# Optimization experiments

Measured on AMD Instinct MI355X. Metric: run time of the kernel, lower is better.

## Reference

```python
import jax, jax.numpy as jnp
import numpy as np

B = 8            # graphs per batch
NP = 1000        # nodes per graph (fixed 1000x1000 connectivity)
N = B * NP       # total nodes
F = 1000         # node feature dim (== NP)
HC = 32          # hidden_channels
NL = 3           # num_layers (HC*NL == 96, the hard-coded bnh dim)
K = 5            # Chebyshev order
HID = 128        # mlp hidden
NC = 2           # num_classes
DEG = 10         # avg degree
E = N * DEG      # total edges
TRI = F * (F - 1) // 2   # 499500 strict-upper-triangle entries
EPS = 1e-5


def setup_inputs():
    ks = jax.random.split(jax.random.key(0), 16)
    x = jax.random.normal(ks[0], (N, F), jnp.float32)  # per-graph connectivity rows
    # block-structured edges: endpoints stay inside their own graph
    offs = jnp.repeat(jnp.arange(B, dtype=jnp.int32) * NP, NP * DEG)
    src = jax.random.randint(ks[1], (E,), 0, NP, jnp.int32) + offs
    dst = jax.random.randint(ks[2], (E,), 0, NP, jnp.int32) + offs
    edge_index = jnp.stack([src, dst])
    batch = jnp.repeat(jnp.arange(B, dtype=jnp.int32), NP)
    nrm = lambda k, shape, s=0.05: jax.random.normal(k, shape, jnp.float32) * s
    return dict(
        x=x, edge_index=edge_index, batch=batch,
        conv_w0=nrm(ks[3], (K, F, HC)), conv_b0=jnp.zeros((HC,), jnp.float32),
        conv_w1=nrm(ks[4], (K, HC, HC)), conv_b1=jnp.zeros((HC,), jnp.float32),
        conv_w2=nrm(ks[5], (K, HC, HC)), conv_b2=jnp.zeros((HC,), jnp.float32),
        bnh_g=jnp.ones((HC * NL,), jnp.float32), bnh_b=jnp.zeros((HC * NL,), jnp.float32),
        bn_g=jnp.ones((TRI,), jnp.float32), bn_b=jnp.zeros((TRI,), jnp.float32),
        mlp_w1=nrm(ks[6], (TRI, HID), 0.002), mlp_b1=jnp.zeros((HID,), jnp.float32),
        bn1_g=jnp.ones((HID,), jnp.float32), bn1_b=jnp.zeros((HID,), jnp.float32),
        mlp_w2=nrm(ks[7], (HID, HID // 2)), mlp_b2=jnp.zeros((HID // 2,), jnp.float32),
        bn2_g=jnp.ones((HID // 2,), jnp.float32), bn2_b=jnp.zeros((HID // 2,), jnp.float32),
        mlp_w3=nrm(ks[8], (HID // 2, HID // 2)), mlp_b3=jnp.zeros((HID // 2,), jnp.float32),
        bn3_g=jnp.ones((HID // 2,), jnp.float32), bn3_b=jnp.zeros((HID // 2,), jnp.float32),
        mlp_w4=nrm(ks[9], (HID // 2, NC)), mlp_b4=jnp.zeros((NC,), jnp.float32),
    )


def _bn(z, g, b):
    # BatchNorm1d in training mode (batch stats, biased var), eps=1e-5
    m = jnp.mean(z, axis=0)
    v = jnp.var(z, axis=0)
    return (z - m) * jax.lax.rsqrt(v + EPS) * g + b


def _cheb(z, src, dst, w, Ws, b):
    # PyG ChebConv with sym norm, lambda_max=2: L~ = -D^{-1/2} A D^{-1/2}
    prop = lambda t: jax.ops.segment_sum(w[:, None] * t[src], dst, num_segments=N)
    Tx0, out = z, z @ Ws[0]
    Tx1 = prop(z)
    out = out + Tx1 @ Ws[1]
    for k in range(2, Ws.shape[0]):
        Tx2 = 2.0 * prop(Tx1) - Tx0
        out = out + Tx2 @ Ws[k]
        Tx0, Tx1 = Tx1, Tx2
    return out + b


def reference(x, edge_index, batch, conv_w0, conv_b0, conv_w1, conv_b1, conv_w2, conv_b2,
              bnh_g, bnh_b, bn_g, bn_b, mlp_w1, mlp_b1, bn1_g, bn1_b,
              mlp_w2, mlp_b2, bn2_g, bn2_b, mlp_w3, mlp_b3, bn3_g, bn3_b, mlp_w4, mlp_b4):
    src, dst = edge_index[0], edge_index[1]
    # symmetric normalization weights (negated scaled Laplacian off-diagonal)
    deg = jax.ops.segment_sum(jnp.ones((E,), x.dtype), src, num_segments=N)
    dinv = jnp.where(deg > 0, deg ** -0.5, 0.0)
    w = -dinv[src] * dinv[dst]
    # node features replaced by tiled identity, as in the original forward
    xid = jnp.tile(jnp.eye(NP, dtype=x.dtype), (B, 1))  # [N, F]
    h1 = jnp.tanh(_cheb(xid, src, dst, w, conv_w0, conv_b0))
    h2 = jnp.tanh(_cheb(h1, src, dst, w, conv_w1, conv_b1))
    h3 = jnp.tanh(_cheb(h2, src, dst, w, conv_w2, conv_b2))
    # MeanAggregation per graph
    cnt = jax.ops.segment_sum(jnp.ones((N,), x.dtype), batch, num_segments=B)[:, None]
    pool = lambda h: jax.ops.segment_sum(h, batch, num_segments=B) / cnt
    emb = jnp.concatenate([pool(h1), pool(h2), pool(h3)], axis=1)  # [B, 96]
    hbn = _bn(emb, bnh_g, bnh_b)
    # static strict-upper-triangle gather (replaces per-graph triu().nonzero())
    rawx = x.reshape(B, F, F)
    iu0, iu1 = np.triu_indices(F, k=1)
    feats = rawx[:, iu0, iu1]                       # [B, 499500]
    fbn = _bn(feats, bn_g, bn_b)
    # MLP (dropout = identity / eval)
    a = jax.nn.relu(_bn(fbn @ mlp_w1 + mlp_b1, bn1_g, bn1_b))
    a = jax.nn.relu(_bn(a @ mlp_w2 + mlp_b2, bn2_g, bn2_b))
    a = jax.nn.relu(_bn(a @ mlp_w3 + mlp_b3, bn3_g, bn3_b))
    logits = a @ mlp_w4 + mlp_b4
    logp = jax.nn.log_softmax(logits, axis=1)
    return logp, hbn
```

## Files before the change

### kernel.cpp

```cpp
#include <hip/hip_runtime.h>

#define NN 8000
#define NPP 1000
#define FF 1000
#define HCC 32
#define KK 5
#define EE 80000
#define EDGB 10000
#define DPAD 40
#define TRIN 499500
#define HID 128
#define EPSV 1e-5f
#define NREP 64

#define IDX_ACC  0
#define IDX_DEGI 65536
#define IDX_FILL 73536
#define IDX_OVC  81536
#define IDX_OVF  81540
#define IDX_EPAD 81920
#define ZERO_N   737280
#define IDX_H1   737280
#define IDX_H2   993280
#define IDX_EMB  1249280


__global__ void k_count(const int* __restrict__ src, int* __restrict__ degi) {
  int e = blockIdx.x * blockDim.x + threadIdx.x;
  if (e >= EE) return;
  atomicAdd(&degi[src[e]], 1);
}

__global__ void k_fillpad(const int* __restrict__ src, const int* __restrict__ dst,
                          const int* __restrict__ degi, int* __restrict__ fill,
                          int2* __restrict__ epad, int* __restrict__ ovc,
                          int4* __restrict__ ovf) {
  int e = blockIdx.x * blockDim.x + threadIdx.x;
  if (e >= EE) return;
  int s = src[e], d = dst[e];
  int dd = degi[d];
  float w = -rsqrtf((float)degi[s]) * ((dd > 0) ? rsqrtf((float)dd) : 0.0f);
  int g = e / EDGB;
  int sl = s - g * NPP;
  int dl = d - g * NPP;
  int pos = atomicAdd(&fill[d], 1);
  if (pos < DPAD) {
    int2 pk;
    pk.x = sl;
    pk.y = __float_as_int(w);
    epad[(size_t)g * (DPAD * 1024) + pos * 1024 + dl] = pk;
  } else {
    int oi = atomicAdd(ovc, 1);
    if (oi < 64) ovf[oi] = make_int4(g, dl, sl, __float_as_int(w));
  }
}

__global__ void __launch_bounds__(1024, 4) k_layer(
    const float* __restrict__ cw, const float* __restrict__ bias,
    const float* __restrict__ hin, float* __restrict__ hout,
    const int2* __restrict__ epad, const int* __restrict__ ovc,
    const int4* __restrict__ ovf,
    float* __restrict__ emb, int L) {
  __shared__ float ckl[KK][NPP];
  __shared__ float bcur[NPP];
  __shared__ float wcol[KK][HCC];
  __shared__ float part[32];
  const int t = threadIdx.x;
  const int g = blockIdx.x >> 5;
  const int c = blockIdx.x & 31;
  const bool act = t < NPP;
  if (hin == nullptr) {
    if (act) {
#pragma unroll
      for (int k = 0; k < KK; ++k)
        ckl[k][t] = cw[k * (FF * HCC) + t * HCC + c];
    }
  } else {
    if (t < KK * HCC) {
      int k = t >> 5, j = t & 31;
      wcol[k][j] = cw[k * (HCC * HCC) + j * HCC + c];
    }
    __syncthreads();
    if (act) {
      float hrow[HCC];
      const float* hp = hin + ((size_t)g * NPP + t) * HCC;
#pragma unroll
      for (int q = 0; q < HCC / 4; ++q) {
        float4 f = *(const float4*)(hp + q * 4);
        hrow[q * 4 + 0] = f.x; hrow[q * 4 + 1] = f.y;
        hrow[q * 4 + 2] = f.z; hrow[q * 4 + 3] = f.w;
      }
#pragma unroll
      for (int k = 0; k < KK; ++k) {
        float a = 0.0f;
#pragma unroll
        for (int j = 0; j < HCC; ++j) a += hrow[j] * wcol[k][j];
        ckl[k][t] = a;
      }
    }
  }
  __syncthreads();
  if (act) bcur[t] = ckl[KK - 1][t];
  float bprev = 0.0f;
  float v = 0.0f;
  __syncthreads();
  const int2* ed = epad + (size_t)g * (DPAD * 1024);
  const int nov = ovc[0];
#pragma unroll
  for (int step = 0; step < 4; ++step) {
    const float alpha = (step == 3) ? 1.0f : 2.0f;
    const int kidx = 3 - step;
    float acc = 0.0f;
#pragma unroll 8
    for (int d = 0; d < DPAD; ++d) {
      int2 pk = ed[d * 1024 + t];
      acc += __int_as_float(pk.y) * bcur[pk.x];
    }
    for (int i = 0; i < nov; ++i) {
      int4 o = ovf[i];
      if (o.x == g && o.y == t) acc += __int_as_float(o.w) * bcur[o.z];
    }
    if (act) v = alpha * acc - bprev + ckl[kidx][t];
    __syncthreads();
    if (act) { bprev = bcur[t]; bcur[t] = v; }
    __syncthreads();
  }
  if (act) {
    float h = tanhf(v + bias[c]);
    if (hout) hout[((size_t)g * NPP + t) * HCC + c] = h;
    bcur[t] = h;
  }
  __syncthreads();
  if (t < 32) {
    float s = 0.0f;
    for (int i = t; i < NPP; i += 32) s += bcur[i];
    part[t] = s;
  }
  __syncthreads();
  if (t == 0) {
    float s = 0.0f;
#pragma unroll
    for (int q = 0; q < 32; ++q) s += part[q];
    emb[g * 96 + L * HCC + c] = s * (1.0f / (float)NPP);
  }
}


__device__ __forceinline__ int tri_S(int i) { return i * 999 - (i * (i - 1)) / 2; }

__global__ void __launch_bounds__(256) k_gemm1(const float* __restrict__ x,
                                               const float* __restrict__ bng,
                                               const float* __restrict__ bnb,
                                               const float* __restrict__ W1,
                                               float* __restrict__ accrep) {
  __shared__ float fbn_s[256][8];
  __shared__ float red[8][128];
  const int tid = threadIdx.x;
  const int c4 = (tid & 31) * 4;
  const int stripe = tid >> 5;
  const int j0 = blockIdx.x * 256;
  float acc[8][4];
#pragma unroll
  for (int b = 0; b < 8; ++b)
#pragma unroll
    for (int q = 0; q < 4; ++q) acc[b][q] = 0.0f;

  {
    const int j = j0 + tid;
    float vals[8];
    if (j < TRIN) {
      const float tt = 1999.0f;
      int i = (int)((tt - sqrtf(tt * tt - 8.0f * (float)j)) * 0.5f);
      i = max(0, min(i, 998));
      while (tri_S(i + 1) <= j) ++i;
      while (tri_S(i) > j) --i;
      int i1 = j - tri_S(i) + i + 1;
      size_t base = (size_t)i * FF + i1;
#pragma unroll
      for (int b = 0; b < 8; ++b) vals[b] = x[(size_t)b * (FF * NPP) + base];
      float m = 0.0f;
#pragma unroll
      for (int b = 0; b < 8; ++b) m += vals[b];
      m *= 0.125f;
      float va = 0.0f;
#pragma unroll
      for (int b = 0; b < 8; ++b) { float d = vals[b] - m; va += d * d; }
      va *= 0.125f;
      float sc = bng[j] * rsqrtf(va + EPSV);
      float tb = bnb[j] - m * sc;
#pragma unroll
      for (int b = 0; b < 8; ++b) vals[b] = sc * vals[b] + tb;
    } else {
#pragma unroll
      for (int b = 0; b < 8; ++b) vals[b] = 0.0f;
    }
    *(float4*)&fbn_s[tid][0] = make_float4(vals[0], vals[1], vals[2], vals[3]);
    *(float4*)&fbn_s[tid][4] = make_float4(vals[4], vals[5], vals[6], vals[7]);
  }
  __syncthreads();

  const int jbase = stripe * 32;
  const int jmax = min(32, TRIN - j0 - jbase);
  const float* wp = W1 + (size_t)(j0 + jbase) * HID + c4;
  if (jmax == 32) {
#pragma unroll 4
    for (int jj = 0; jj < 32; ++jj) {
      float4 w = *(const float4*)(wp + (size_t)jj * HID);
      float4 f0 = *(const float4*)&fbn_s[jbase + jj][0];
      float4 f1 = *(const float4*)&fbn_s[jbase + jj][4];
      float wv[4] = {w.x, w.y, w.z, w.w};
      float fv[8] = {f0.x, f0.y, f0.z, f0.w, f1.x, f1.y, f1.z, f1.w};
#pragma unroll
      for (int b = 0; b < 8; ++b)
#pragma unroll
        for (int q = 0; q < 4; ++q) acc[b][q] += fv[b] * wv[q];
    }
  } else {
    for (int jj = 0; jj < jmax; ++jj) {
      float4 w = *(const float4*)(wp + (size_t)jj * HID);
      float4 f0 = *(const float4*)&fbn_s[jbase + jj][0];
      float4 f1 = *(const float4*)&fbn_s[jbase + jj][4];
      float wv[4] = {w.x, w.y, w.z, w.w};
      float fv[8] = {f0.x, f0.y, f0.z, f0.w, f1.x, f1.y, f1.z, f1.w};
#pragma unroll
      for (int b = 0; b < 8; ++b)
#pragma unroll
        for (int q = 0; q < 4; ++q) acc[b][q] += fv[b] * wv[q];
    }
  }
#pragma unroll
  for (int b = 0; b < 8; ++b) {
    __syncthreads();
    red[stripe][c4 + 0] = acc[b][0];
    red[stripe][c4 + 1] = acc[b][1];
    red[stripe][c4 + 2] = acc[b][2];
    red[stripe][c4 + 3] = acc[b][3];
    __syncthreads();
    if (tid < 128) {
      float s = 0.0f;
#pragma unroll
      for (int q = 0; q < 8; ++q) s += red[q][tid];
      atomicAdd(&accrep[(blockIdx.x & (NREP - 1)) * 1024 + b * HID + tid], s);
    }
  }
}


__global__ void __launch_bounds__(1024) k_mlp(
    const float* __restrict__ accrep, const float* __restrict__ emb,
    const float* __restrict__ hg, const float* __restrict__ hb,
    const float* __restrict__ mb1,
    const float* __restrict__ g1, const float* __restrict__ be1,
    const float* __restrict__ W2, const float* __restrict__ mb2,
    const float* __restrict__ g2, const float* __restrict__ be2,
    const float* __restrict__ W3, const float* __restrict__ mb3,
    const float* __restrict__ g3, const float* __restrict__ be3,
    const float* __restrict__ W4, const float* __restrict__ mb4,
    float* __restrict__ out) {
  __shared__ float A[8][128];
  __shared__ float V[8][128];
  __shared__ float Bm[8][64];
  __shared__ float Cm[8][64];
  __shared__ float lg[8][2];
  const int tid = threadIdx.x;
  if (tid < 96) {
    float v[8];
    float m = 0.0f;
#pragma unroll
    for (int q = 0; q < 8; ++q) { v[q] = emb[q * 96 + tid]; m += v[q]; }
    m *= 0.125f;
    float va = 0.0f;
#pragma unroll
    for (int q = 0; q < 8; ++q) { float d = v[q] - m; va += d * d; }
    va *= 0.125f;
    float s = hg[tid] * rsqrtf(va + EPSV);
    float t = hb[tid] - m * s;
#pragma unroll
    for (int q = 0; q < 8; ++q) out[16 + q * 96 + tid] = s * v[q] + t;
  }
  {
    const int c = tid & 127;
    const int b = tid >> 7;
    float a = mb1[c];
#pragma unroll 8
    for (int rep = 0; rep < NREP; ++rep) a += accrep[rep * 1024 + tid];
    V[b][c] = a;
  }
  __syncthreads();
  {
    const int c = tid & 127;
    const int b = tid >> 7;
    float m = 0.0f;
#pragma unroll
    for (int q = 0; q < 8; ++q) m += V[q][c];
    m *= 0.125f;
    float va = 0.0f;
#pragma unroll
    for (int q = 0; q < 8; ++q) { float d = V[q][c] - m; va += d * d; }
    va *= 0.125f;
    float s = g1[c] * rsqrtf(va + EPSV);
    float t = be1[c] - m * s;
    float z = s * V[b][c] + t;
    A[b][c] = (z > 0.0f) ? z : 0.0f;
  }
  __syncthreads();
  if (tid < 512) {
    const int c = tid & 63;
    const int b = tid >> 6;
    float a = mb2[c];
    for (int j = 0; j < 128; ++j) a += A[b][j] * W2[j * 64 + c];
    V[b][c] = a;
  }
  __syncthreads();
  if (tid < 512) {
    const int c = tid & 63;
    const int b = tid >> 6;
    float m = 0.0f;
#pragma unroll
    for (int q = 0; q < 8; ++q) m += V[q][c];
    m *= 0.125f;
    float va = 0.0f;
#pragma unroll
    for (int q = 0; q < 8; ++q) { float d = V[q][c] - m; va += d * d; }
    va *= 0.125f;
    float s = g2[c] * rsqrtf(va + EPSV);
    float t = be2[c] - m * s;
    float z = s * V[b][c] + t;
    Bm[b][c] = (z > 0.0f) ? z : 0.0f;
  }
  __syncthreads();
  if (tid < 512) {
    const int c = tid & 63;
    const int b = tid >> 6;
    float a = mb3[c];
    for (int j = 0; j < 64; ++j) a += Bm[b][j] * W3[j * 64 + c];
    V[b][c] = a;
  }
  __syncthreads();
  if (tid < 512) {
    const int c = tid & 63;
    const int b = tid >> 6;
    float m = 0.0f;
#pragma unroll
    for (int q = 0; q < 8; ++q) m += V[q][c];
    m *= 0.125f;
    float va = 0.0f;
#pragma unroll
    for (int q = 0; q < 8; ++q) { float d = V[q][c] - m; va += d * d; }
    va *= 0.125f;
    float s = g3[c] * rsqrtf(va + EPSV);
    float t = be3[c] - m * s;
    float z = s * V[b][c] + t;
    Cm[b][c] = (z > 0.0f) ? z : 0.0f;
  }
  __syncthreads();
  if (tid < 16) {
    int b = tid >> 1, c = tid & 1;
    float a4 = mb4[c];
    for (int j = 0; j < 64; ++j) a4 += Cm[b][j] * W4[j * 2 + c];
    lg[b][c] = a4;
  }
  __syncthreads();
  if (tid < 8) {
    float l0 = lg[tid][0], l1 = lg[tid][1];
    float mm = fmaxf(l0, l1);
    float lse = mm + logf(expf(l0 - mm) + expf(l1 - mm));
    out[tid * 2 + 0] = l0 - lse;
    out[tid * 2 + 1] = l1 - lse;
  }
}


extern "C" void kernel_launch(void* const* d_in, const int* in_sizes, int n_in,
                              void* d_out, int out_size, void* d_ws, size_t ws_size,
                              hipStream_t stream) {
  const float* x = (const float*)d_in[0];
  const int* ei = (const int*)d_in[1];
  const int* src = ei;
  const int* dst = ei + EE;
  const float* cw0 = (const float*)d_in[3];
  const float* cb0 = (const float*)d_in[4];
  const float* cw1 = (const float*)d_in[5];
  const float* cb1 = (const float*)d_in[6];
  const float* cw2 = (const float*)d_in[7];
  const float* cb2 = (const float*)d_in[8];
  const float* bnhg = (const float*)d_in[9];
  const float* bnhb = (const float*)d_in[10];
  const float* bng = (const float*)d_in[11];
  const float* bnb = (const float*)d_in[12];
  const float* mw1 = (const float*)d_in[13];
  const float* mb1 = (const float*)d_in[14];
  const float* b1g = (const float*)d_in[15];
  const float* b1b = (const float*)d_in[16];
  const float* mw2 = (const float*)d_in[17];
  const float* mb2 = (const float*)d_in[18];
  const float* b2g = (const float*)d_in[19];
  const float* b2b = (const float*)d_in[20];
  const float* mw3 = (const float*)d_in[21];
  const float* mb3 = (const float*)d_in[22];
  const float* b3g = (const float*)d_in[23];
  const float* b3b = (const float*)d_in[24];
  const float* mw4 = (const float*)d_in[25];
  const float* mb4 = (const float*)d_in[26];

  float* ws = (float*)d_ws;
  int* wsi = (int*)d_ws;
  float* out = (float*)d_out;

  float* accrep = ws + IDX_ACC;
  int* degi = wsi + IDX_DEGI;
  int* fill = wsi + IDX_FILL;
  int* ovc = wsi + IDX_OVC;
  int4* ovf = (int4*)(wsi + IDX_OVF);
  int2* epad = (int2*)(wsi + IDX_EPAD);
  float* h1 = ws + IDX_H1;
  float* h2 = ws + IDX_H2;
  float* emb = ws + IDX_EMB;

  hipMemsetAsync(wsi, 0, ZERO_N * sizeof(int), stream);

  k_gemm1<<<(TRIN + 255) / 256, 256, 0, stream>>>(x, bng, bnb, mw1, accrep);
  k_count<<<(EE + 255) / 256, 256, 0, stream>>>(src, degi);
  k_fillpad<<<(EE + 255) / 256, 256, 0, stream>>>(src, dst, degi, fill, epad, ovc, ovf);
  k_layer<<<256, 1024, 0, stream>>>(cw0, cb0, nullptr, h1, epad, ovc, ovf, emb, 0);
  k_layer<<<256, 1024, 0, stream>>>(cw1, cb1, h1, h2, epad, ovc, ovf, emb, 1);
  k_layer<<<256, 1024, 0, stream>>>(cw2, cb2, h2, nullptr, epad, ovc, ovf, emb, 2);
  k_mlp<<<1, 1024, 0, stream>>>(accrep, emb, bnhg, bnhb, mb1, b1g, b1b,
                                mw2, mb2, b2g, b2b, mw3, mb3, b3g, b3b,
                                mw4, mb4, out);
}
```

Baseline: 524.0 us.

## Keep padded edge lists and Chebyshev coefficients in registers; shrink padding

Edge padding per destination drops from 40 to 24 slots, with a larger overflow buffer (256) for the rare nodes above that. Each thread now loads its padded edge list and Chebyshev coefficients into registers once and reuses them over all four recurrence steps, instead of reading global memory every step and keeping coefficients in shared memory. The launch bound is relaxed to 2 blocks per SM for the extra registers, and one barrier is dropped on the last step. Separately, the MLP weight stream uses nontemporal loads; the trade-off is lower occupancy and a longer linear scan of the overflow list each step if many nodes overflow.

```diff
diff --git a/kernel.cpp b/kernel.cpp
--- a/kernel.cpp
+++ b/kernel.cpp
@@ -7,22 +7,25 @@
 #define KK 5
 #define EE 80000
 #define EDGB 10000
-#define DPAD 40
+#define DPAD 24
+#define OVCAP 256
 #define TRIN 499500
 #define HID 128
 #define EPSV 1e-5f
 #define NREP 64
+
+typedef float fvec4 __attribute__((ext_vector_type(4)));
 
 #define IDX_ACC  0
 #define IDX_DEGI 65536
 #define IDX_FILL 73536
 #define IDX_OVC  81536
 #define IDX_OVF  81540
-#define IDX_EPAD 81920
-#define ZERO_N   737280
-#define IDX_H1   737280
-#define IDX_H2   993280
-#define IDX_EMB  1249280
+#define IDX_EPAD 82564
+#define ZERO_N   475780
+#define IDX_H1   475780
+#define IDX_H2   731780
+#define IDX_EMB  987780
 
 
 __global__ void k_count(const int* __restrict__ src, int* __restrict__ degi) {
@@ -51,17 +54,16 @@
     epad[(size_t)g * (DPAD * 1024) + pos * 1024 + dl] = pk;
   } else {
     int oi = atomicAdd(ovc, 1);
-    if (oi < 64) ovf[oi] = make_int4(g, dl, sl, __float_as_int(w));
-  }
-}
-
-__global__ void __launch_bounds__(1024, 4) k_layer(
+    if (oi < OVCAP) ovf[oi] = make_int4(g, dl, sl, __float_as_int(w));
+  }
+}
+
+__global__ void __launch_bounds__(1024, 2) k_layer(
     const float* __restrict__ cw, const float* __restrict__ bias,
     const float* __restrict__ hin, float* __restrict__ hout,
     const int2* __restrict__ epad, const int* __restrict__ ovc,
     const int4* __restrict__ ovf,
     float* __restrict__ emb, int L) {
-  __shared__ float ckl[KK][NPP];
   __shared__ float bcur[NPP];
   __shared__ float wcol[KK][HCC];
   __shared__ float part[32];
@@ -69,64 +71,65 @@
   const int g = blockIdx.x >> 5;
   const int c = blockIdx.x & 31;
   const bool act = t < NPP;
+  const int tn = act ? t : 0;
+  float ck[KK];
   if (hin == nullptr) {
-    if (act) {
-#pragma unroll
-      for (int k = 0; k < KK; ++k)
-        ckl[k][t] = cw[k * (FF * HCC) + t * HCC + c];
-    }
+#pragma unroll
+    for (int k = 0; k < KK; ++k)
+      ck[k] = cw[k * (FF * HCC) + tn * HCC + c];
   } else {
     if (t < KK * HCC) {
       int k = t >> 5, j = t & 31;
       wcol[k][j] = cw[k * (HCC * HCC) + j * HCC + c];
     }
     __syncthreads();
-    if (act) {
-      float hrow[HCC];
-      const float* hp = hin + ((size_t)g * NPP + t) * HCC;
-#pragma unroll
-      for (int q = 0; q < HCC / 4; ++q) {
-        float4 f = *(const float4*)(hp + q * 4);
-        hrow[q * 4 + 0] = f.x; hrow[q * 4 + 1] = f.y;
-        hrow[q * 4 + 2] = f.z; hrow[q * 4 + 3] = f.w;
-      }
-#pragma unroll
-      for (int k = 0; k < KK; ++k) {
-        float a = 0.0f;
-#pragma unroll
-        for (int j = 0; j < HCC; ++j) a += hrow[j] * wcol[k][j];
-        ckl[k][t] = a;
-      }
-    }
-  }
-  __syncthreads();
-  if (act) bcur[t] = ckl[KK - 1][t];
+    float hrow[HCC];
+    const float* hp = hin + ((size_t)g * NPP + tn) * HCC;
+#pragma unroll
+    for (int q = 0; q < HCC / 4; ++q) {
+      float4 f = *(const float4*)(hp + q * 4);
+      hrow[q * 4 + 0] = f.x; hrow[q * 4 + 1] = f.y;
+      hrow[q * 4 + 2] = f.z; hrow[q * 4 + 3] = f.w;
+    }
+#pragma unroll
+    for (int k = 0; k < KK; ++k) {
+      float a = 0.0f;
+#pragma unroll
+      for (int j = 0; j < HCC; ++j) a += hrow[j] * wcol[k][j];
+      ck[k] = a;
+    }
+  }
+  int2 ereg[DPAD];
+  const int2* ed = epad + (size_t)g * (DPAD * 1024);
+#pragma unroll
+  for (int d = 0; d < DPAD; ++d) ereg[d] = ed[d * 1024 + t];
+  int nov = ovc[0];
+  if (nov > OVCAP) nov = OVCAP;
+  if (act) bcur[t] = ck[KK - 1];
   float bprev = 0.0f;
   float v = 0.0f;
   __syncthreads();
-  const int2* ed = epad + (size_t)g * (DPAD * 1024);
-  const int nov = ovc[0];
 #pragma unroll
   for (int step = 0; step < 4; ++step) {
     const float alpha = (step == 3) ? 1.0f : 2.0f;
     const int kidx = 3 - step;
     float acc = 0.0f;
-#pragma unroll 8
-    for (int d = 0; d < DPAD; ++d) {
-      int2 pk = ed[d * 1024 + t];
-      acc += __int_as_float(pk.y) * bcur[pk.x];
-    }
+#pragma unroll
+    for (int d = 0; d < DPAD; ++d)
+      acc += __int_as_float(ereg[d].y) * bcur[ereg[d].x];
     for (int i = 0; i < nov; ++i) {
       int4 o = ovf[i];
       if (o.x == g && o.y == t) acc += __int_as_float(o.w) * bcur[o.z];
     }
-    if (act) v = alpha * acc - bprev + ckl[kidx][t];
+    v = alpha * acc - bprev + ck[kidx];
     __syncthreads();
-    if (act) { bprev = bcur[t]; bcur[t] = v; }
-    __syncthreads();
-  }
+    if (step < 3) {
+      if (act) { bprev = bcur[t]; bcur[t] = v; }
+      __syncthreads();
+    }
+  }
+  float h = tanhf(v + bias[c]);
   if (act) {
-    float h = tanhf(v + bias[c]);
     if (hout) hout[((size_t)g * NPP + t) * HCC + c] = h;
     bcur[t] = h;
   }
@@ -205,7 +208,7 @@
   if (jmax == 32) {
 #pragma unroll 4
     for (int jj = 0; jj < 32; ++jj) {
-      float4 w = *(const float4*)(wp + (size_t)jj * HID);
+      fvec4 w = __builtin_nontemporal_load((const fvec4*)(wp + (size_t)jj * HID));
       float4 f0 = *(const float4*)&fbn_s[jbase + jj][0];
       float4 f1 = *(const float4*)&fbn_s[jbase + jj][4];
       float wv[4] = {w.x, w.y, w.z, w.w};
@@ -217,7 +220,7 @@
     }
   } else {
     for (int jj = 0; jj < jmax; ++jj) {
-      float4 w = *(const float4*)(wp + (size_t)jj * HID);
+      fvec4 w = __builtin_nontemporal_load((const fvec4*)(wp + (size_t)jj * HID));
       float4 f0 = *(const float4*)&fbn_s[jbase + jj][0];
       float4 f1 = *(const float4*)&fbn_s[jbase + jj][4];
       float wv[4] = {w.x, w.y, w.z, w.w};
```

Result: faster. 468.0 us (-10.7%).
